# Performance work log

Measured on AMD Instinct MI355X. Metric: run time of the kernel, lower is better.

The kernel has to match this reference:

```python
import jax, jax.numpy as jnp
import numpy as np

NUM_LEVELS = 4
RADIUS = 4


def _avg_pool2(x):
    # F.avg_pool2d(x, 2, stride=2) for even H, W
    B, D, H, W = x.shape
    return x.reshape(B, D, H // 2, 2, W // 2, 2).mean(axis=(3, 5))


def _local_corr(f1, f2, coords, radius):
    # f1, f2: (B, D, H, W); coords: (B, 2, H, W) pixel coords into f2
    B, D, H, W = f1.shape
    offs = jnp.arange(-radius, radius + 1, dtype=coords.dtype)
    dx, dy = jnp.meshgrid(offs, offs, indexing='ij')  # x slow, y fast (as in _get_local_grids)
    dx = dx.reshape(-1)
    dy = dy.reshape(-1)  # (K,) with K=(2r+1)^2
    x = coords[:, 0][..., None] + dx  # (B,H,W,K)
    y = coords[:, 1][..., None] + dy
    # grid_sample(padding_mode='border', align_corners=True) == clamp coords then bilinear
    x = jnp.clip(x, 0.0, W - 1.0)
    y = jnp.clip(y, 0.0, H - 1.0)
    x0 = jnp.floor(x)
    y0 = jnp.floor(y)
    x1 = jnp.minimum(x0 + 1.0, W - 1.0)
    y1 = jnp.minimum(y0 + 1.0, H - 1.0)
    wx1 = x - x0
    wx0 = 1.0 - wx1
    wy1 = y - y0
    wy0 = 1.0 - wy1
    f2f = f2.reshape(B, D, H * W)

    def corner(xc, yc, w):
        idx = (yc * W + xc).astype(jnp.int32).reshape(B, -1)  # (B, H*W*K)
        g = jax.vmap(lambda f, i: jnp.take(f, i, axis=1))(f2f, idx)  # (B,D,H*W*K)
        g = g.reshape(B, D, H, W, -1)  # (B,D,H,W,K)
        # per-pixel dot over feature dim, weighted by bilinear weight
        return w * jnp.einsum('bdhw,bdhwk->bhwk', f1, g)

    corr = (corner(x0, y0, wx0 * wy0) + corner(x1, y0, wx1 * wy0)
            + corner(x0, y1, wx0 * wy1) + corner(x1, y1, wx1 * wy1))
    corr = corr / jnp.sqrt(jnp.asarray(D, dtype=corr.dtype))
    return jnp.transpose(corr, (0, 3, 1, 2))  # (B,K,H,W)


def _corr_pyramid(fmap1, fmap2, coords):
    p1, p2 = [fmap1], [fmap2]
    for _ in range(NUM_LEVELS - 1):
        p1.append(_avg_pool2(p1[-1]))
        p2.append(_avg_pool2(p2[-1]))
    outs = []
    B = coords.shape[0]
    for i in range(NUM_LEVELS):
        Hl, Wl = p1[i].shape[2], p1[i].shape[3]
        if i == 0:
            c = coords
        else:
            c = jax.image.resize(coords, (B, 2, Hl, Wl), method='linear')
        c = c / (2.0 ** i)  # coords / scale, per level
        outs.append(_local_corr(p1[i], p2[i], c, RADIUS))
    return tuple(outs)


def setup_inputs() -> dict:
    key = jax.random.key(0)
    k1, k2, k3 = jax.random.split(key, 3)
    B, D, H, W = 1, 128, 64, 96
    fmap1 = jax.random.normal(k1, (B, D, H, W), dtype=jnp.float32)
    fmap2 = jax.random.normal(k2, (B, D, H, W), dtype=jnp.float32)
    yy, xx = jnp.meshgrid(jnp.arange(H, dtype=jnp.float32),
                          jnp.arange(W, dtype=jnp.float32), indexing='ij')
    base = jnp.stack([xx, yy], axis=0)[None]  # (1,2,H,W), coords_grid order (x,y)
    flow = 3.0 * jax.random.normal(k3, (B, 2, H, W), dtype=jnp.float32)
    coords = base + flow
    return {"fmap1": fmap1, "fmap2": fmap2, "coords": coords}


def reference(fmap1, fmap2, coords):
    return _corr_pyramid(fmap1, fmap2, coords)
```

## Files before the change

kernel.cpp:

```cpp
#include <hip/hip_runtime.h>
#include <hip/hip_fp16.h>

#define D 128
#define H0 64
#define W0 96
#define HW0 6144
#define INV_SQRT_D 0.08838834764831843f

#define H_F1T0 0
#define H_F1T1 786432
#define H_F1T2 983040
#define H_F1T3 1032192
#define H_F2T0 1048576
#define H_F2T1 1835008
#define H_F2T2 2031616
#define H_F2T3 2080768

#define OUT_L0 0
#define OUT_L1 497664
#define OUT_L2 622080
#define OUT_L3 653184

typedef _Float16 h2 __attribute__((ext_vector_type(2)));
union F4H { float4 f; h2 h[4]; };

__device__ __forceinline__ float dot2f(h2 a, h2 b, float c) {
#if __has_builtin(__builtin_amdgcn_fdot2)
    return __builtin_amdgcn_fdot2(a, b, c, false);
#else
    return c + (float)a.x * (float)b.x + (float)a.y * (float)b.y;
#endif
}

__device__ __forceinline__ void gp_to_level(int gp, int& level, int& p) {
    if (gp < 6144)      { level = 0; p = gp; }
    else if (gp < 7680) { level = 1; p = gp - 6144; }
    else if (gp < 8064) { level = 2; p = gp - 7680; }
    else                { level = 3; p = gp - 8064; }
}

__global__ __launch_bounds__(512) void k_prep(const float* __restrict__ f1,
                                              const float* __restrict__ f2,
                                              float* __restrict__ ws) {
    const int b = blockIdx.x;
    const int t = threadIdx.x;
    _Float16* wh = (_Float16*)ws;
    __shared__ float T[64 * 33];
    const int m  = b / 384;
    const int r  = b - m * 384;
    const int tix = r >> 2;
    const int dq  = r & 3;
    const int tr = tix / 12, tc = tix - (tix / 12) * 12;
    const float* in = (m ? f2 : f1) + dq * 32 * HW0;

    {
        const int dl  = t >> 4;
        const int row = (t >> 1) & 7;
        const int c4  = t & 1;
        float4 v = *(const float4*)(in + dl * HW0 + (tr * 8 + row) * W0
                                    + tc * 8 + c4 * 4);
        const int l0 = row * 8 + c4 * 4;
        T[(l0 + 0) * 33 + dl] = v.x;
        T[(l0 + 1) * 33 + dl] = v.y;
        T[(l0 + 2) * 33 + dl] = v.z;
        T[(l0 + 3) * 33 + dl] = v.w;
    }
    __syncthreads();

    {
        _Float16* o0 = wh + (m ? H_F2T0 : H_F1T0) + dq * 32;
        h2* o0h = (h2*)o0;
#pragma unroll
        for (int pass = 0; pass < 2; ++pass) {
            int idx = t + pass * 512;
            int pl = idx >> 4, c2 = idx & 15;
            h2 hv;
            hv.x = (_Float16)T[pl * 33 + 2 * c2];
            hv.y = (_Float16)T[pl * 33 + 2 * c2 + 1];
            int gp = (tr * 8 + (pl >> 3)) * W0 + tc * 8 + (pl & 7);
            o0h[gp * 64 + c2] = hv;
        }
    }
    {
        _Float16* o1 = wh + (m ? H_F2T1 : H_F1T1) + dq * 32;
        int d = t & 31, p1 = t >> 5;
        int i1 = p1 >> 2, j1 = p1 & 3;
        int l00 = (i1 * 2) * 8 + j1 * 2;
        float v = T[l00 * 33 + d] + T[(l00 + 1) * 33 + d]
                + T[(l00 + 8) * 33 + d] + T[(l00 + 9) * 33 + d];
        o1[((tr * 4 + i1) * 48 + tc * 4 + j1) * D + d] = (_Float16)(0.25f * v);
    }
    if (t < 128) {
        _Float16* o2 = wh + (m ? H_F2T2 : H_F1T2) + dq * 32;
        int d = t & 31, p2 = t >> 5;
        int i2 = p2 >> 1, j2 = p2 & 1;
        float acc = 0.0f;
#pragma unroll
        for (int a = 0; a < 4; ++a)
#pragma unroll
            for (int c2 = 0; c2 < 4; ++c2)
                acc += T[((i2 * 4 + a) * 8 + j2 * 4 + c2) * 33 + d];
        o2[((tr * 2 + i2) * 24 + tc * 2 + j2) * D + d] = (_Float16)(acc * 0.0625f);
    }
    if (t < 32) {
        _Float16* o3 = wh + (m ? H_F2T3 : H_F1T3) + dq * 32;
        float acc = 0.0f;
        for (int l2 = 0; l2 < 64; ++l2) acc += T[l2 * 33 + t];
        o3[(tr * 12 + tc) * D + t] = (_Float16)(acc * 0.015625f);
    }
}

__global__ __launch_bounds__(1024, 8) void k_dc(const float* __restrict__ coords0,
                                                const float* __restrict__ ws,
                                                float* __restrict__ out) {
    __shared__ float Gs[16 * 101];
    __shared__ float cxs[16], cys[16];
    const _Float16* wh = (const _Float16*)ws;

    const int t = threadIdx.x;
    const int w = t >> 6;
    const int ln = t & 63;
    const int oct = ln >> 3;
    const int sub = ln & 7;

    const int gp0 = blockIdx.x * 16;
    const int gp = gp0 + w;

    int level, p;
    gp_to_level(gp, level, p);
    const int Hl = H0 >> level, Wl = W0 >> level;

    const int f1offs[4] = {H_F1T0, H_F1T1, H_F1T2, H_F1T3};
    const int f2offs[4] = {H_F2T0, H_F2T1, H_F2T2, H_F2T3};
    const int outoffs[4] = {OUT_L0, OUT_L1, OUT_L2, OUT_L3};

    const _Float16* f2t = wh + f2offs[level];

    const _Float16* f1p = wh + f1offs[level] + p * D + sub * 8;
    F4H a0f, a1f;
    a0f.f = *(const float4*)(f1p);
    a1f.f = *(const float4*)(f1p + 64);

    float cx, cy;
    if (level == 0) {
        cx = coords0[p];
        cy = coords0[HW0 + p];
    } else {
        const int ho = p / Wl, wo = p - (p / Wl) * Wl;
        const float ff = (float)(1 << level);
        const float sfy = (ho + 0.5f) * ff - 0.5f;
        const float sfx = (wo + 0.5f) * ff - 0.5f;
        int ylo = max(0, (int)ceilf(sfy - ff));
        int yhi = min(H0 - 1, (int)floorf(sfy + ff));
        int xlo = max(0, (int)ceilf(sfx - ff));
        int xhi = min(W0 - 1, (int)floorf(sfx + ff));
        int nx = xhi - xlo + 1;
        int nt = (yhi - ylo + 1) * nx;
        float a0 = 0.0f, a1 = 0.0f, wsum = 0.0f;
        for (int i = ln; i < nt; i += 64) {
            int ry = i / nx, rx = i - ry * nx;
            int iy = ylo + ry, ix = xlo + rx;
            float wy = fmaxf(1.0f - fabsf(sfy - (float)iy) / ff, 0.0f);
            float wx = fmaxf(1.0f - fabsf(sfx - (float)ix) / ff, 0.0f);
            float wgt = wy * wx;
            wsum += wgt;
            a0 += wgt * coords0[iy * W0 + ix];
            a1 += wgt * coords0[HW0 + iy * W0 + ix];
        }
#pragma unroll
        for (int off = 32; off; off >>= 1) {
            a0 += __shfl_xor(a0, off);
            a1 += __shfl_xor(a1, off);
            wsum += __shfl_xor(wsum, off);
        }
        cx = a0 / wsum / ff;
        cy = a1 / wsum / ff;
    }
    if (ln == 0) { cxs[w] = cx; cys[w] = cy; }
    const int fx = (int)floorf(cx), fy = (int)floorf(cy);
    const int shf = 5 - level;

#pragma unroll 2
    for (int i = 0; i < 13; ++i) {
        int g = i * 8 + oct;
        int gc = min(g, 99);
        int gy = (gc * 205) >> 11;
        int gx = gc - gy * 10;
        int iy = min(max(fy - 4 + gy, 0), Hl - 1);
        int ix = min(max(fx - 4 + gx, 0), Wl - 1);
        int rowp = ((iy * 3) << shf) + ix;
        const _Float16* row = f2t + rowp * D + sub * 8;
        F4H v0, v1;
        v0.f = *(const float4*)(row);
        v1.f = *(const float4*)(row + 64);
        float s = 0.0f;
        s = dot2f(a0f.h[0], v0.h[0], s);
        s = dot2f(a0f.h[1], v0.h[1], s);
        s = dot2f(a0f.h[2], v0.h[2], s);
        s = dot2f(a0f.h[3], v0.h[3], s);
        s = dot2f(a1f.h[0], v1.h[0], s);
        s = dot2f(a1f.h[1], v1.h[1], s);
        s = dot2f(a1f.h[2], v1.h[2], s);
        s = dot2f(a1f.h[3], v1.h[3], s);
        s += __shfl_xor(s, 1);
        s += __shfl_xor(s, 2);
        s += __shfl_xor(s, 4);
        if (sub == 0 && g < 100) Gs[w * 101 + g] = s;
    }
    __syncthreads();

    {
        const int px = t & 15;
        const int kk = t >> 4;
        int lv0, p0;
        gp_to_level(gp0, lv0, p0);
        const int Hb = H0 >> lv0, Wb = W0 >> lv0;
        const int npb = Hb * Wb;
        float* outp = out + outoffs[lv0] + p0 + px;
        const float bx = cxs[px], by = cys[px];
        const float Wm1 = (float)(Wb - 1), Hm1 = (float)(Hb - 1);
        const float* Gp = &Gs[px * 101];

        for (int k = kk; k < 81; k += 64) {
            int dxi = (k * 57) >> 9;
            int dyi = k - dxi * 9;
            float x = fminf(fmaxf(bx + (float)(dxi - 4), 0.0f), Wm1);
            float y = fminf(fmaxf(by + (float)(dyi - 4), 0.0f), Hm1);
            float wx1 = x - floorf(x), wx0 = 1.0f - wx1;
            float wy1 = y - floorf(y), wy0 = 1.0f - wy1;
            int g00 = dyi * 10 + dxi;
            float v = wx0 * wy0 * Gp[g00]      + wx1 * wy0 * Gp[g00 + 1]
                    + wx0 * wy1 * Gp[g00 + 10] + wx1 * wy1 * Gp[g00 + 11];
            outp[k * npb] = v * INV_SQRT_D;
        }
    }
}

extern "C" void kernel_launch(void* const* d_in, const int* in_sizes, int n_in,
                              void* d_out, int out_size, void* d_ws, size_t ws_size,
                              hipStream_t stream) {
    const float* fmap1  = (const float*)d_in[0];
    const float* fmap2  = (const float*)d_in[1];
    const float* coords = (const float*)d_in[2];
    float* out = (float*)d_out;
    float* ws = (float*)d_ws;

    k_prep<<<dim3(768), dim3(512), 0, stream>>>(fmap1, fmap2, ws);
    k_dc<<<dim3(510), dim3(1024), 0, stream>>>(coords, ws, out);
}
```

Measured before the change: 78.45 us.

## Fuse prep and correlation kernels into one cooperative launch with grid sync

Combines the feature-prep/pooling kernel and the correlation kernel into a single cooperative kernel. A grid-wide barrier separates the two phases, which removes one kernel launch and its gap. The correlation work is re-split into 512-thread blocks of 8 pixels each, so 1020 tasks run over 768 blocks in a persistent loop. If the cooperative launch fails, it falls back to two launches, at the cost of grid-sync overhead and an uneven second round of tasks.

```diff
diff --git a/kernel.cpp b/kernel.cpp
--- a/kernel.cpp
+++ b/kernel.cpp
@@ -1,5 +1,8 @@
 #include <hip/hip_runtime.h>
 #include <hip/hip_fp16.h>
+#include <hip/hip_cooperative_groups.h>
+
+namespace cg = cooperative_groups;
 
 #define D 128
 #define H0 64
@@ -39,13 +42,21 @@
     else                { level = 3; p = gp - 8064; }
 }
 
-__global__ __launch_bounds__(512) void k_prep(const float* __restrict__ f1,
-                                              const float* __restrict__ f2,
-                                              float* __restrict__ ws) {
-    const int b = blockIdx.x;
-    const int t = threadIdx.x;
-    _Float16* wh = (_Float16*)ws;
-    __shared__ float T[64 * 33];
+__device__ __forceinline__ int f1off(int l) {
+    return l == 0 ? H_F1T0 : l == 1 ? H_F1T1 : l == 2 ? H_F1T2 : H_F1T3;
+}
+__device__ __forceinline__ int f2off(int l) {
+    return l == 0 ? H_F2T0 : l == 1 ? H_F2T1 : l == 2 ? H_F2T2 : H_F2T3;
+}
+__device__ __forceinline__ int outoff(int l) {
+    return l == 0 ? OUT_L0 : l == 1 ? OUT_L1 : l == 2 ? OUT_L2 : OUT_L3;
+}
+
+__device__ __forceinline__ void prep_body(int b, int t,
+                                          const float* __restrict__ f1,
+                                          const float* __restrict__ f2,
+                                          _Float16* __restrict__ wh,
+                                          float* __restrict__ T) {
     const int m  = b / 384;
     const int r  = b - m * 384;
     const int tix = r >> 2;
@@ -110,33 +121,27 @@
     }
 }
 
-__global__ __launch_bounds__(1024, 8) void k_dc(const float* __restrict__ coords0,
-                                                const float* __restrict__ ws,
-                                                float* __restrict__ out) {
-    __shared__ float Gs[16 * 101];
-    __shared__ float cxs[16], cys[16];
-    const _Float16* wh = (const _Float16*)ws;
-
-    const int t = threadIdx.x;
+__device__ __forceinline__ void dc_task(int task, int t,
+                                        const float* __restrict__ coords0,
+                                        const _Float16* __restrict__ wh,
+                                        float* __restrict__ out,
+                                        float* __restrict__ Gs,
+                                        float* __restrict__ cxs,
+                                        float* __restrict__ cys) {
     const int w = t >> 6;
     const int ln = t & 63;
     const int oct = ln >> 3;
     const int sub = ln & 7;
 
-    const int gp0 = blockIdx.x * 16;
+    const int gp0 = task * 8;
     const int gp = gp0 + w;
 
     int level, p;
     gp_to_level(gp, level, p);
     const int Hl = H0 >> level, Wl = W0 >> level;
-
-    const int f1offs[4] = {H_F1T0, H_F1T1, H_F1T2, H_F1T3};
-    const int f2offs[4] = {H_F2T0, H_F2T1, H_F2T2, H_F2T3};
-    const int outoffs[4] = {OUT_L0, OUT_L1, OUT_L2, OUT_L3};
-
-    const _Float16* f2t = wh + f2offs[level];
-
-    const _Float16* f1p = wh + f1offs[level] + p * D + sub * 8;
+    const _Float16* f2t = wh + f2off(level);
+
+    const _Float16* f1p = wh + f1off(level) + p * D + sub * 8;
     F4H a0f, a1f;
     a0f.f = *(const float4*)(f1p);
     a1f.f = *(const float4*)(f1p + 64);
@@ -210,13 +215,13 @@
     __syncthreads();
 
     {
-        const int px = t & 15;
-        const int kk = t >> 4;
+        const int px = t & 7;
+        const int kk = t >> 3;
         int lv0, p0;
         gp_to_level(gp0, lv0, p0);
         const int Hb = H0 >> lv0, Wb = W0 >> lv0;
         const int npb = Hb * Wb;
-        float* outp = out + outoffs[lv0] + p0 + px;
+        float* outp = out + outoff(lv0) + p0 + px;
         const float bx = cxs[px], by = cys[px];
         const float Wm1 = (float)(Wb - 1), Hm1 = (float)(Hb - 1);
         const float* Gp = &Gs[px * 101];
@@ -236,6 +241,42 @@
     }
 }
 
+__global__ __launch_bounds__(512, 6) void k_fused(const float* __restrict__ f1,
+                                                  const float* __restrict__ f2,
+                                                  const float* __restrict__ coords0,
+                                                  float* __restrict__ ws,
+                                                  float* __restrict__ out) {
+    __shared__ float T[64 * 33];
+    __shared__ float Gs[8 * 101];
+    __shared__ float cxs[8], cys[8];
+    _Float16* wh = (_Float16*)ws;
+
+    prep_body(blockIdx.x, threadIdx.x, f1, f2, wh, T);
+
+    __threadfence();
+    cg::this_grid().sync();
+
+    for (int task = blockIdx.x; task < 1020; task += 768) {
+        dc_task(task, threadIdx.x, coords0, (const _Float16*)wh, out, Gs, cxs, cys);
+        __syncthreads();
+    }
+}
+
+__global__ __launch_bounds__(512) void k_prep(const float* __restrict__ f1,
+                                              const float* __restrict__ f2,
+                                              float* __restrict__ ws) {
+    __shared__ float T[64 * 33];
+    prep_body(blockIdx.x, threadIdx.x, f1, f2, (_Float16*)ws, T);
+}
+
+__global__ __launch_bounds__(512, 6) void k_dc8(const float* __restrict__ coords0,
+                                                const float* __restrict__ ws,
+                                                float* __restrict__ out) {
+    __shared__ float Gs[8 * 101];
+    __shared__ float cxs[8], cys[8];
+    dc_task(blockIdx.x, threadIdx.x, coords0, (const _Float16*)ws, out, Gs, cxs, cys);
+}
+
 extern "C" void kernel_launch(void* const* d_in, const int* in_sizes, int n_in,
                               void* d_out, int out_size, void* d_ws, size_t ws_size,
                               hipStream_t stream) {
@@ -245,6 +286,12 @@
     float* out = (float*)d_out;
     float* ws = (float*)d_ws;
 
-    k_prep<<<dim3(768), dim3(512), 0, stream>>>(fmap1, fmap2, ws);
-    k_dc<<<dim3(510), dim3(1024), 0, stream>>>(coords, ws, out);
-}
+    void* args[] = { (void*)&fmap1, (void*)&fmap2, (void*)&coords,
+                     (void*)&ws, (void*)&out };
+    hipError_t err = hipLaunchCooperativeKernel(k_fused, dim3(768), dim3(512),
+                                                args, 0, stream);
+    if (err != hipSuccess) {
+        k_prep<<<dim3(768), dim3(512), 0, stream>>>(fmap1, fmap2, ws);
+        k_dc8<<<dim3(1020), dim3(512), 0, stream>>>(coords, ws, out);
+    }
+}
```

Result: slower. 252.0 us (+221.3%).

## Shrink correlation blocks to four waves and batch all gather loads before dots

Applied to the files above, without the earlier changes.

The correlation kernel moves from 1024-thread blocks covering 16 pixels to 256-thread blocks covering 4 pixels, with four times as many blocks. The 13-step gather loop is split so all offsets are computed first, then all 26 vector loads are issued, then the dot products run. This aims to raise memory-level parallelism and reduce barrier stalls. It costs much higher register pressure, and a lower occupancy hint that may limit latency hiding. Per-level offset arrays become inline select functions.

```diff
diff --git a/kernel.cpp b/kernel.cpp
--- a/kernel.cpp
+++ b/kernel.cpp
@@ -37,6 +37,16 @@
     else if (gp < 7680) { level = 1; p = gp - 6144; }
     else if (gp < 8064) { level = 2; p = gp - 7680; }
     else                { level = 3; p = gp - 8064; }
+}
+
+__device__ __forceinline__ int f1off(int l) {
+    return l == 0 ? H_F1T0 : l == 1 ? H_F1T1 : l == 2 ? H_F1T2 : H_F1T3;
+}
+__device__ __forceinline__ int f2off(int l) {
+    return l == 0 ? H_F2T0 : l == 1 ? H_F2T1 : l == 2 ? H_F2T2 : H_F2T3;
+}
+__device__ __forceinline__ int outoff(int l) {
+    return l == 0 ? OUT_L0 : l == 1 ? OUT_L1 : l == 2 ? OUT_L2 : OUT_L3;
 }
 
 __global__ __launch_bounds__(512) void k_prep(const float* __restrict__ f1,
@@ -110,11 +120,11 @@
     }
 }
 
-__global__ __launch_bounds__(1024, 8) void k_dc(const float* __restrict__ coords0,
+__global__ __launch_bounds__(256, 3) void k_dc4(const float* __restrict__ coords0,
                                                 const float* __restrict__ ws,
                                                 float* __restrict__ out) {
-    __shared__ float Gs[16 * 101];
-    __shared__ float cxs[16], cys[16];
+    __shared__ float Gs[4 * 101];
+    __shared__ float cxs[4], cys[4];
     const _Float16* wh = (const _Float16*)ws;
 
     const int t = threadIdx.x;
@@ -123,20 +133,14 @@
     const int oct = ln >> 3;
     const int sub = ln & 7;
 
-    const int gp0 = blockIdx.x * 16;
+    const int gp0 = blockIdx.x * 4;
     const int gp = gp0 + w;
 
     int level, p;
     gp_to_level(gp, level, p);
     const int Hl = H0 >> level, Wl = W0 >> level;
 
-    const int f1offs[4] = {H_F1T0, H_F1T1, H_F1T2, H_F1T3};
-    const int f2offs[4] = {H_F2T0, H_F2T1, H_F2T2, H_F2T3};
-    const int outoffs[4] = {OUT_L0, OUT_L1, OUT_L2, OUT_L3};
-
-    const _Float16* f2t = wh + f2offs[level];
-
-    const _Float16* f1p = wh + f1offs[level] + p * D + sub * 8;
+    const _Float16* f1p = wh + f1off(level) + p * D + sub * 8;
     F4H a0f, a1f;
     a0f.f = *(const float4*)(f1p);
     a1f.f = *(const float4*)(f1p + 64);
@@ -180,7 +184,9 @@
     const int fx = (int)floorf(cx), fy = (int)floorf(cy);
     const int shf = 5 - level;
 
-#pragma unroll 2
+    const _Float16* base = wh + f2off(level) + sub * 8;
+    int off16[13];
+#pragma unroll
     for (int i = 0; i < 13; ++i) {
         int g = i * 8 + oct;
         int gc = min(g, 99);
@@ -188,35 +194,43 @@
         int gx = gc - gy * 10;
         int iy = min(max(fy - 4 + gy, 0), Hl - 1);
         int ix = min(max(fx - 4 + gx, 0), Wl - 1);
-        int rowp = ((iy * 3) << shf) + ix;
-        const _Float16* row = f2t + rowp * D + sub * 8;
-        F4H v0, v1;
-        v0.f = *(const float4*)(row);
-        v1.f = *(const float4*)(row + 64);
+        off16[i] = ((((iy * 3) << shf) + ix) << 7);
+    }
+
+    F4H v0[13], v1[13];
+#pragma unroll
+    for (int i = 0; i < 13; ++i) {
+        v0[i].f = *(const float4*)(base + off16[i]);
+        v1[i].f = *(const float4*)(base + off16[i] + 64);
+    }
+
+#pragma unroll
+    for (int i = 0; i < 13; ++i) {
         float s = 0.0f;
-        s = dot2f(a0f.h[0], v0.h[0], s);
-        s = dot2f(a0f.h[1], v0.h[1], s);
-        s = dot2f(a0f.h[2], v0.h[2], s);
-        s = dot2f(a0f.h[3], v0.h[3], s);
-        s = dot2f(a1f.h[0], v1.h[0], s);
-        s = dot2f(a1f.h[1], v1.h[1], s);
-        s = dot2f(a1f.h[2], v1.h[2], s);
-        s = dot2f(a1f.h[3], v1.h[3], s);
+        s = dot2f(a0f.h[0], v0[i].h[0], s);
+        s = dot2f(a0f.h[1], v0[i].h[1], s);
+        s = dot2f(a0f.h[2], v0[i].h[2], s);
+        s = dot2f(a0f.h[3], v0[i].h[3], s);
+        s = dot2f(a1f.h[0], v1[i].h[0], s);
+        s = dot2f(a1f.h[1], v1[i].h[1], s);
+        s = dot2f(a1f.h[2], v1[i].h[2], s);
+        s = dot2f(a1f.h[3], v1[i].h[3], s);
         s += __shfl_xor(s, 1);
         s += __shfl_xor(s, 2);
         s += __shfl_xor(s, 4);
+        int g = i * 8 + oct;
         if (sub == 0 && g < 100) Gs[w * 101 + g] = s;
     }
     __syncthreads();
 
     {
-        const int px = t & 15;
-        const int kk = t >> 4;
+        const int px = t & 3;
+        const int kk = t >> 2;
         int lv0, p0;
         gp_to_level(gp0, lv0, p0);
         const int Hb = H0 >> lv0, Wb = W0 >> lv0;
         const int npb = Hb * Wb;
-        float* outp = out + outoffs[lv0] + p0 + px;
+        float* outp = out + outoff(lv0) + p0 + px;
         const float bx = cxs[px], by = cys[px];
         const float Wm1 = (float)(Wb - 1), Hm1 = (float)(Hb - 1);
         const float* Gp = &Gs[px * 101];
@@ -246,5 +260,5 @@
     float* ws = (float*)d_ws;
 
     k_prep<<<dim3(768), dim3(512), 0, stream>>>(fmap1, fmap2, ws);
-    k_dc<<<dim3(510), dim3(1024), 0, stream>>>(coords, ws, out);
-}
+    k_dc4<<<dim3(2040), dim3(256), 0, stream>>>(coords, ws, out);
+}
```

Result: no change. 78.44 us (-0.0%).
